# Performance work log

Hardware: AMD Instinct MI355X
Metric: run time of the kernel (lower is better)

The kernel has to match this reference:

```python
import jax, jax.numpy as jnp
import numpy as np

EPS = 1e-5

def _ln(x, g, b):
    m = x.mean(-1, keepdims=True)
    v = x.var(-1, keepdims=True)
    return (x - m) / jnp.sqrt(v + EPS) * g + b

def _dwconv(x, w, b, stride, pad):
    # x: [B,C,H,W], w: [C,1,k,k] depthwise
    C = x.shape[1]
    y = jax.lax.conv_general_dilated(
        x, w, (stride, stride), pad,
        feature_group_count=C,
        dimension_numbers=('NCHW', 'OIHW', 'NCHW'))
    return y + b[None, :, None, None]

def setup_inputs() -> dict:
    key = jax.random.key(0)
    ks = jax.random.split(key, 16)
    B, H, W, C = 8, 64, 64, 256
    N = H * W
    sr = 8
    d = {}
    d['x'] = jax.random.normal(ks[0], (B, N, C), jnp.float32)
    d['q_w'] = jax.random.normal(ks[1], (C, C), jnp.float32) * 0.02
    d['kv1_w'] = jax.random.normal(ks[2], (C, C), jnp.float32) * 0.02
    d['kv2_w'] = jax.random.normal(ks[3], (C, C), jnp.float32) * 0.02
    d['proj_w'] = jax.random.normal(ks[4], (C, C), jnp.float32) * 0.02
    d['proj_b'] = jnp.zeros((C,), jnp.float32)
    k1 = sr // 2
    d['sr1_w'] = jax.random.normal(ks[5], (C, 1, k1, k1), jnp.float32) * np.sqrt(2.0 / (k1 * k1))
    d['sr1_b'] = jnp.zeros((C,), jnp.float32)
    d['sr2_w'] = jax.random.normal(ks[6], (C, 1, sr, sr), jnp.float32) * np.sqrt(2.0 / (sr * sr))
    d['sr2_b'] = jnp.zeros((C,), jnp.float32)
    d['ln1_g'] = jnp.ones((C,), jnp.float32)
    d['ln1_b'] = jnp.zeros((C,), jnp.float32)
    d['ln2_g'] = jnp.ones((C,), jnp.float32)
    d['ln2_b'] = jnp.zeros((C,), jnp.float32)
    d['lc1_w'] = jax.random.normal(ks[7], (C // 2, 1, 3, 3), jnp.float32) * np.sqrt(2.0 / 9.0)
    d['lc1_b'] = jnp.zeros((C // 2,), jnp.float32)
    d['lc2_w'] = jax.random.normal(ks[8], (C // 2, 1, 3, 3), jnp.float32) * np.sqrt(2.0 / 9.0)
    d['lc2_b'] = jnp.zeros((C // 2,), jnp.float32)
    d['H'] = H
    d['W'] = W
    return d

def reference(x, q_w, kv1_w, kv2_w, proj_w, proj_b,
              sr1_w, sr1_b, sr2_w, sr2_b,
              ln1_g, ln1_b, ln2_g, ln2_b,
              lc1_w, lc1_b, lc2_w, lc2_b, H, W):
    B, N, C = x.shape
    nh = 8
    nh2 = nh // 2
    hd = C // nh
    sr = 8
    scale = hd ** -0.5

    # q: [B, nh, N, hd]
    q = jnp.einsum('bnc,dc->bnd', x, q_w).reshape(B, N, nh, hd).transpose(0, 2, 1, 3)

    x_ = x.transpose(0, 2, 1).reshape(B, C, H, W)
    x1 = _dwconv(x_, sr1_w, sr1_b, sr // 2, 'VALID')            # [B,C,H/4,W/4]
    x1 = x1.reshape(B, C, -1).transpose(0, 2, 1)                 # [B,N1,C]
    x1 = jax.nn.gelu(_ln(x1, ln1_g, ln1_b), approximate=False)
    x2 = _dwconv(x_, sr2_w, sr2_b, sr, 'VALID')                  # [B,C,H/8,W/8]
    x2 = x2.reshape(B, C, -1).transpose(0, 2, 1)                 # [B,N2,C]
    x2 = jax.nn.gelu(_ln(x2, ln2_g, ln2_b), approximate=False)

    def branch(xr, kv_w, qh, Hs, Ws, lc_w, lc_b):
        Bn, Ns, _ = xr.shape
        kv = jnp.einsum('bnc,dc->bnd', xr, kv_w).reshape(Bn, Ns, 2, nh2, hd).transpose(2, 0, 3, 1, 4)
        k, v = kv[0], kv[1]                                      # [B,nh2,Ns,hd]
        attn = jax.nn.softmax(jnp.einsum('bhqd,bhkd->bhqk', qh, k) * scale, axis=-1)
        # depthwise local conv injected into v
        v_sp = v.transpose(0, 2, 1, 3).reshape(Bn, Ns, C // 2).transpose(0, 2, 1).reshape(Bn, C // 2, Hs, Ws)
        v_lc = _dwconv(v_sp, lc_w, lc_b, 1, ((1, 1), (1, 1)))
        v = v + v_lc.reshape(Bn, nh2, hd, Ns).transpose(0, 1, 3, 2)
        out = jnp.einsum('bhqk,bhkd->bhqd', attn, v)             # [B,nh2,N,hd]
        return out.transpose(0, 2, 1, 3).reshape(Bn, N, C // 2)

    o1 = branch(x1, kv1_w, q[:, :nh2], H * 2 // sr, W * 2 // sr, lc1_w, lc1_b)
    o2 = branch(x2, kv2_w, q[:, nh2:], H // sr, W // sr, lc2_w, lc2_b)
    out = jnp.concatenate([o1, o2], axis=-1)
    return jnp.einsum('bnc,dc->bnd', out, proj_w) + proj_b
```

## Files before the change

kernel.cpp:

```cpp
#include <hip/hip_runtime.h>
#include <math.h>

static constexpr int Bb  = 8;
static constexpr int Nn  = 4096;
static constexpr int Cc  = 256;
static constexpr int N1c = 256;
static constexpr int N2c = 64;

typedef __attribute__((ext_vector_type(8))) _Float16 f16x8;
typedef __attribute__((ext_vector_type(4))) _Float16 f16x4;
typedef __attribute__((ext_vector_type(4))) float    f32x4v;

__global__ __launch_bounds__(256)
void prep_down(const float* __restrict__ w0, const float* __restrict__ w1,
               const float* __restrict__ w2, const float* __restrict__ w3,
               const float* __restrict__ x,
               const float* __restrict__ sr1w, const float* __restrict__ b1,
               const float* __restrict__ g1,   const float* __restrict__ lb1,
               const float* __restrict__ sr2w, const float* __restrict__ b2,
               const float* __restrict__ g2,   const float* __restrict__ lb2,
               _Float16* __restrict__ wf, _Float16* __restrict__ x1o,
               _Float16* __restrict__ x2o) {
  const int bid = blockIdx.x, c = threadIdx.x;
  if (bid < 256) {
    const int wsel = bid >> 6;
    const float* w = wsel == 0 ? w0 : wsel == 1 ? w1 : wsel == 2 ? w2 : w3;
    const int i = ((bid & 63) * 256 + c) * 4;
    float4 v = *(const float4*)(w + i);
    f16x4 o = {(_Float16)v.x, (_Float16)v.y, (_Float16)v.z, (_Float16)v.w};
    *(f16x4*)(wf + (size_t)wsel * 65536 + i) = o;
    return;
  }
  const int t = bid - 256;
  const int b = t >> 6, n2 = t & 63;
  const int i2 = n2 >> 3, j2 = n2 & 7;
  const int lane = c & 63, wave = c >> 6;
  const float* xb = x + ((size_t)b * Nn) * Cc + c;

  float w1r[16];
#pragma unroll
  for (int q = 0; q < 4; ++q)
    *(float4*)&w1r[4 * q] = *(const float4*)(sr1w + c * 16 + 4 * q);

  float a2 = b2[c];
  float a1[2][2] = {{b1[c], b1[c]}, {b1[c], b1[c]}};
#pragma unroll
  for (int dy = 0; dy < 8; ++dy) {
    float vr[8], w2r[8];
    *(float4*)&w2r[0] = *(const float4*)(sr2w + c * 64 + dy * 8);
    *(float4*)&w2r[4] = *(const float4*)(sr2w + c * 64 + dy * 8 + 4);
#pragma unroll
    for (int dx = 0; dx < 8; ++dx)
      vr[dx] = xb[(size_t)((8 * i2 + dy) * 64 + 8 * j2 + dx) * 256];
#pragma unroll
    for (int dx = 0; dx < 8; ++dx) {
      a2 = fmaf(w2r[dx], vr[dx], a2);
      a1[dy >> 2][dx >> 2] = fmaf(w1r[(dy & 3) * 4 + (dx & 3)], vr[dx],
                                  a1[dy >> 2][dx >> 2]);
    }
  }
  float vals[5] = {a2, a1[0][0], a1[0][1], a1[1][0], a1[1][1]};
  __shared__ float redS[4][5], redQ[4][5];
#pragma unroll
  for (int p = 0; p < 5; ++p) {
    float s = vals[p], q2 = vals[p] * vals[p];
#pragma unroll
    for (int off = 1; off < 64; off <<= 1) {
      s  += __shfl_xor(s, off);
      q2 += __shfl_xor(q2, off);
    }
    if (lane == 0) { redS[wave][p] = s; redQ[wave][p] = q2; }
  }
  __syncthreads();
#pragma unroll
  for (int p = 0; p < 5; ++p) {
    const float sum = redS[0][p] + redS[1][p] + redS[2][p] + redS[3][p];
    const float sq  = redQ[0][p] + redQ[1][p] + redQ[2][p] + redQ[3][p];
    const float mean = sum * (1.f / Cc);
    const float var  = sq * (1.f / Cc) - mean * mean;
    const float gg = (p == 0) ? g2[c] : g1[c];
    const float bb = (p == 0) ? lb2[c] : lb1[c];
    const float xn = (vals[p] - mean) * rsqrtf(var + 1e-5f) * gg + bb;
    const float gel = 0.5f * xn * (1.f + erff(xn * 0.70710678118654752440f));
    if (p == 0) {
      x2o[((size_t)b * N2c + n2) * 256 + c] = (_Float16)gel;
    } else {
      const int a = (p - 1) >> 1, bbx = (p - 1) & 1;
      const int n1 = (2 * i2 + a) * 16 + (2 * j2 + bbx);
      x1o[((size_t)b * N1c + n1) * 256 + c] = (_Float16)gel;
    }
  }
}

struct GemmSmem { _Float16 Asl[2][64][40]; _Float16 Bsl[2][256][40]; };

template<int AM, int OM, bool BIAS>
__device__ __forceinline__
void gemm_body(GemmSmem& sm, const void* __restrict__ Ain,
               const _Float16* __restrict__ Wf, const float* __restrict__ bias,
               void* __restrict__ Outv, int m0) {
  const int tid = threadIdx.x, lane = tid & 63, wid = tid >> 6;
  const int qi = lane & 15, g = lane >> 4;
  const int ar = tid >> 2, ak = (tid & 3) * 8;
  const int arow = m0 + ar;

  const float*    pa32 = (const float*)Ain + (size_t)arow * 256 + ak;
  const _Float16* pa16f = (const _Float16*)Ain + (size_t)arow * 256 + ak;
  const _Float16* pa16h = (const _Float16*)Ain
      + ((size_t)(arow >> 12) * 8 * 4096 + (arow & 4095)) * 32 + ak;
  const _Float16* pw = Wf + (size_t)tid * 256;

  f32x4v acc[4][4] = {};
  f16x8 rA; f16x8 rB[4];

#define LDREG(k0)                                                          \
  do {                                                                     \
    if (AM == 0) {                                                         \
      float4 t0 = *(const float4*)(pa32 + (k0));                           \
      float4 t1 = *(const float4*)(pa32 + (k0) + 4);                       \
      rA = (f16x8){(_Float16)t0.x, (_Float16)t0.y, (_Float16)t0.z,         \
                   (_Float16)t0.w, (_Float16)t1.x, (_Float16)t1.y,         \
                   (_Float16)t1.z, (_Float16)t1.w};                        \
    } else if (AM == 1) {                                                  \
      rA = *(const f16x8*)(pa16f + (k0));                                  \
    } else {                                                               \
      rA = *(const f16x8*)(pa16h + (size_t)((k0) >> 5) * 131072);          \
    }                                                                      \
    _Pragma("unroll")                                                      \
    for (int i = 0; i < 4; ++i) rB[i] = *(const f16x8*)(pw + (k0) + i * 8);\
  } while (0)

#define DSWRITE(buf)                                                       \
  do {                                                                     \
    *(f16x8*)&sm.Asl[buf][ar][ak] = rA;                                    \
    _Pragma("unroll")                                                      \
    for (int i = 0; i < 4; ++i) *(f16x8*)&sm.Bsl[buf][tid][i * 8] = rB[i]; \
  } while (0)

  LDREG(0);
  DSWRITE(0);
  LDREG(32);
  __syncthreads();

#pragma unroll
  for (int ks = 0; ks < 8; ++ks) {
    const int cur = ks & 1;
    if (ks < 7) DSWRITE(cur ^ 1);
    if (ks < 6) LDREG((ks + 2) * 32);
    f16x8 af[4], bf[4];
#pragma unroll
    for (int mt = 0; mt < 4; ++mt)
      af[mt] = *(const f16x8*)&sm.Asl[cur][mt * 16 + qi][g * 8];
#pragma unroll
    for (int nt = 0; nt < 4; ++nt)
      bf[nt] = *(const f16x8*)&sm.Bsl[cur][wid * 64 + nt * 16 + qi][g * 8];
#pragma unroll
    for (int nt = 0; nt < 4; ++nt)
#pragma unroll
      for (int mt = 0; mt < 4; ++mt)
        acc[mt][nt] = __builtin_amdgcn_mfma_f32_16x16x32_f16(af[mt], bf[nt], acc[mt][nt], 0, 0, 0);
    __syncthreads();
  }
#undef LDREG
#undef DSWRITE

#pragma unroll
  for (int nt = 0; nt < 4; ++nt) {
    const int col = wid * 64 + nt * 16 + qi;
    const float bv = BIAS ? bias[col] : 0.f;
    const int hs = col >> 5, d = col & 31;
#pragma unroll
    for (int mt = 0; mt < 4; ++mt) {
#pragma unroll
      for (int r = 0; r < 4; ++r) {
        const int row = m0 + mt * 16 + g * 4 + r;
        const float v = acc[mt][nt][r];
        if (OM == 0) {
          ((float*)Outv)[(size_t)row * 256 + col] = v + bv;
        } else if (OM == 1) {
          ((_Float16*)Outv)[((size_t)((row >> 12) * 8 + hs) * 4096 + (row & 4095)) * 32 + d] = (_Float16)v;
        } else if (OM == 2) {
          ((_Float16*)Outv)[((size_t)((row >> 8) * 8 + hs) * 256 + (row & 255)) * 32 + d] = (_Float16)v;
        } else {
          ((_Float16*)Outv)[((size_t)((row >> 6) * 8 + hs) * 64 + (row & 63)) * 32 + d] = (_Float16)v;
        }
      }
    }
  }
}

__global__ __launch_bounds__(256)
void gemms_qkv(const float* __restrict__ x, const _Float16* __restrict__ x1h,
               const _Float16* __restrict__ x2h, const _Float16* __restrict__ wf,
               _Float16* __restrict__ qh, _Float16* __restrict__ kv1,
               _Float16* __restrict__ kv2) {
  __shared__ GemmSmem sm;
  const int bx = blockIdx.x;
  if (bx < 512)      gemm_body<0, 1, false>(sm, x,   wf,             nullptr, qh,  bx * 64);
  else if (bx < 544) gemm_body<1, 2, false>(sm, x1h, wf + 65536,     nullptr, kv1, (bx - 512) * 64);
  else               gemm_body<1, 3, false>(sm, x2h, wf + 2 * 65536, nullptr, kv2, (bx - 544) * 64);
}

__global__ __launch_bounds__(256)
void gemm_proj(const _Float16* __restrict__ qh, const _Float16* __restrict__ wf,
               const float* __restrict__ bias, float* __restrict__ out) {
  __shared__ GemmSmem sm;
  gemm_body<2, 0, true>(sm, qh, wf, bias, out, blockIdx.x * 64);
}

template<int NS, int HS>
__device__ __forceinline__
void attn_body(char* smem, _Float16* __restrict__ qh, const _Float16* __restrict__ kvh,
               const float* __restrict__ lcw, const float* __restrict__ lcb,
               int qc, int b, int h, int hg) {
  constexpr int NT = NS / 16, NC = NS / 32, PS = NS + 8;
  constexpr float KC = 0.17677669529663688f * 1.4426950408889634f;
  _Float16 (*Klds)[40] = (_Float16(*)[40])smem;
  _Float16 (*Vt)[PS]   = (_Float16(*)[PS])(smem + (size_t)NS * 40 * 2);
  _Float16* PlBase     = (_Float16*)(smem + (size_t)NS * 40 * 2 + (size_t)32 * PS * 2);
  _Float16 (*vraw)[32] = (_Float16(*)[32])PlBase;

  const int tid = threadIdx.x, lane = tid & 63, wid = tid >> 6;
  const int g = lane >> 4, qi = lane & 15;

  const _Float16* kp0 = kvh + ((size_t)(b * 8 + h) * NS) * 32;
  const _Float16* vp0 = kvh + ((size_t)(b * 8 + 4 + h) * NS) * 32;
  for (int r = tid; r < NS; r += 256) {
#pragma unroll
    for (int i = 0; i < 4; ++i)
      *(f16x8*)&Klds[r][8 * i] = *(const f16x8*)(kp0 + (size_t)r * 32 + 8 * i);
#pragma unroll
    for (int i = 0; i < 4; ++i)
      *(f16x8*)&vraw[r][8 * i] = *(const f16x8*)(vp0 + (size_t)r * 32 + 8 * i);
  }
  __syncthreads();

  {
    const int d = tid & 31, rg = tid >> 5;
    const int cc = h * 32 + d;
    float wreg[9];
#pragma unroll
    for (int q = 0; q < 9; ++q) wreg[q] = lcw[cc * 9 + q];
    const float bv = lcb[cc];
    for (int r0 = rg; r0 < NS; r0 += 8) {
      const int i = r0 / HS, j = r0 % HS;
      float acc = bv;
#pragma unroll
      for (int dy = 0; dy < 3; ++dy) {
        const int ii = i + dy - 1;
        if (ii < 0 || ii >= HS) continue;
#pragma unroll
        for (int dx = 0; dx < 3; ++dx) {
          const int jj = j + dx - 1;
          if (jj < 0 || jj >= HS) continue;
          acc = fmaf(wreg[dy * 3 + dx], (float)vraw[ii * HS + jj][d], acc);
        }
      }
      Vt[d][r0] = (_Float16)((float)vraw[r0][d] + acc);
    }
  }
  __syncthreads();

  f16x8 vt[2][NC];
#pragma unroll
  for (int dt = 0; dt < 2; ++dt)
#pragma unroll
    for (int c = 0; c < NC; ++c)
      vt[dt][c] = *(const f16x8*)&Vt[16 * dt + qi][32 * c + 8 * g];

  _Float16* Pw = PlBase + (size_t)(wid * 16 + qi) * PS;
  _Float16* qbase = qh + ((size_t)(b * 8 + hg) * 4096) * 32;

  for (int qt = 0; qt < 4; ++qt) {
    const int qrow = qc * 256 + wid * 64 + qt * 16 + qi;
    _Float16* qp = qbase + (size_t)qrow * 32;
    f16x8 qfrag = *(const f16x8*)(qp + 8 * g);
    f32x4v s[NT];
#pragma unroll
    for (int t = 0; t < NT; ++t) {
      f16x8 kf = *(const f16x8*)&Klds[16 * t + qi][8 * g];
      s[t] = __builtin_amdgcn_mfma_f32_16x16x32_f16(kf, qfrag,
                                                    (f32x4v){0.f, 0.f, 0.f, 0.f}, 0, 0, 0);
    }
    float m = s[0][0];
#pragma unroll
    for (int t = 0; t < NT; ++t)
      m = fmaxf(m, fmaxf(fmaxf(s[t][0], s[t][1]), fmaxf(s[t][2], s[t][3])));
    m = fmaxf(m, __shfl_xor(m, 16));
    m = fmaxf(m, __shfl_xor(m, 32));
    float l = 0.f;
#pragma unroll
    for (int t = 0; t < NT; ++t)
#pragma unroll
      for (int r = 0; r < 4; ++r) {
        float p = exp2f((s[t][r] - m) * KC);
        s[t][r] = p; l += p;
      }
    l += __shfl_xor(l, 16);
    l += __shfl_xor(l, 32);
#pragma unroll
    for (int t = 0; t < NT; ++t) {
      f16x4 pw = {(_Float16)s[t][0], (_Float16)s[t][1],
                  (_Float16)s[t][2], (_Float16)s[t][3]};
      *(f16x4*)&Pw[16 * t + 4 * g] = pw;
    }
    f32x4v o0 = {0.f, 0.f, 0.f, 0.f}, o1 = {0.f, 0.f, 0.f, 0.f};
#pragma unroll
    for (int c = 0; c < NC; ++c) {
      f16x8 pf = *(const f16x8*)&Pw[32 * c + 8 * g];
      o0 = __builtin_amdgcn_mfma_f32_16x16x32_f16(vt[0][c], pf, o0, 0, 0, 0);
      o1 = __builtin_amdgcn_mfma_f32_16x16x32_f16(vt[1][c], pf, o1, 0, 0, 0);
    }
    const float inv = 1.f / l;
    f16x4 O0 = {(_Float16)(o0[0] * inv), (_Float16)(o0[1] * inv),
                (_Float16)(o0[2] * inv), (_Float16)(o0[3] * inv)};
    f16x4 O1 = {(_Float16)(o1[0] * inv), (_Float16)(o1[1] * inv),
                (_Float16)(o1[2] * inv), (_Float16)(o1[3] * inv)};
    *(f16x4*)(qp + 4 * g)      = O0;
    *(f16x4*)(qp + 16 + 4 * g) = O1;
  }
}

__global__ __launch_bounds__(256, 2)
void attn_all(_Float16* __restrict__ qh,
              const _Float16* __restrict__ kv1, const _Float16* __restrict__ kv2,
              const float* __restrict__ lc1w, const float* __restrict__ lc1b,
              const float* __restrict__ lc2w, const float* __restrict__ lc2b) {
  __shared__ __align__(16) char smem[71168];
  const int z = blockIdx.z;
  const int b = z >> 1, br = z & 1;
  const int h = blockIdx.y;
  if (br == 0) attn_body<256, 16>(smem, qh, kv1, lc1w, lc1b, blockIdx.x, b, h, h);
  else         attn_body<64,  8>(smem, qh, kv2, lc2w, lc2b, blockIdx.x, b, h, 4 + h);
}

extern "C" void kernel_launch(void* const* d_in, const int* in_sizes, int n_in,
                              void* d_out, int out_size, void* d_ws, size_t ws_size,
                              hipStream_t stream) {
  const float* x      = (const float*)d_in[0];
  const float* q_w    = (const float*)d_in[1];
  const float* kv1_w  = (const float*)d_in[2];
  const float* kv2_w  = (const float*)d_in[3];
  const float* proj_w = (const float*)d_in[4];
  const float* proj_b = (const float*)d_in[5];
  const float* sr1_w  = (const float*)d_in[6];
  const float* sr1_b  = (const float*)d_in[7];
  const float* sr2_w  = (const float*)d_in[8];
  const float* sr2_b  = (const float*)d_in[9];
  const float* ln1_g  = (const float*)d_in[10];
  const float* ln1_b  = (const float*)d_in[11];
  const float* ln2_g  = (const float*)d_in[12];
  const float* ln2_b  = (const float*)d_in[13];
  const float* lc1_w  = (const float*)d_in[14];
  const float* lc1_b  = (const float*)d_in[15];
  const float* lc2_w  = (const float*)d_in[16];
  const float* lc2_b  = (const float*)d_in[17];
  float* out = (float*)d_out;

  _Float16* wf   = (_Float16*)d_ws;
  _Float16* qh   = wf + (size_t)4 * 65536;
  _Float16* x1h  = qh + (size_t)Bb * Nn * Cc;
  _Float16* x2h  = x1h + (size_t)Bb * N1c * Cc;
  _Float16* kv1h = x2h + (size_t)Bb * N2c * Cc;
  _Float16* kv2h = kv1h + (size_t)Bb * N1c * Cc;

  prep_down<<<768, 256, 0, stream>>>(q_w, kv1_w, kv2_w, proj_w, x,
                                     sr1_w, sr1_b, ln1_g, ln1_b,
                                     sr2_w, sr2_b, ln2_g, ln2_b,
                                     wf, x1h, x2h);
  gemms_qkv<<<552, 256, 0, stream>>>(x, x1h, x2h, wf, qh, kv1h, kv2h);
  attn_all<<<dim3(16, 4, 16), 256, 0, stream>>>(qh, kv1h, kv2h,
                                                lc1_w, lc1_b, lc2_w, lc2_b);
  gemm_proj<<<512, 256, 0, stream>>>(qh, wf + 3 * 65536, proj_b, out);
}
```

Before: 106.1 us.

## Precompute depthwise-conv V transpose in separate kernel, shrink attention LDS

Moves the 3x3 depthwise local conv on V, plus its transpose, out of every attention block into a small dedicated kernel that writes a transposed V buffer to global memory once per (batch, head). Previously each of the 16 query-chunk blocks recomputed the same conv. The attention kernel now just loads the precomputed Vt, aliases the P buffer over Vt after an extra barrier, and cuts shared memory from about 71KB to 54KB so it can raise the occupancy hint to 3 blocks. The cost is an extra kernel launch and an extra global round trip for V.

```diff
diff --git a/kernel.cpp b/kernel.cpp
--- a/kernel.cpp
+++ b/kernel.cpp
@@ -210,53 +210,79 @@
 
 template<int NS, int HS>
 __device__ __forceinline__
+void vconvt_body(const _Float16* __restrict__ kvh, const float* __restrict__ lcw,
+                 const float* __restrict__ lcb, _Float16* __restrict__ vtg,
+                 int b, int h, int rbase) {
+  const int tid = threadIdx.x;
+  const int r = rbase + (tid >> 2), dp = tid & 3, d0 = dp * 8;
+  const int i = r / HS, j = r % HS;
+  const _Float16* vsrc = kvh + ((size_t)(b * 8 + 4 + h) * NS) * 32;
+  const float* wb = lcw + (h * 32 + d0) * 9;
+  float acc[8];
+#pragma unroll
+  for (int e = 0; e < 8; ++e) acc[e] = lcb[h * 32 + d0 + e];
+#pragma unroll
+  for (int dy = 0; dy < 3; ++dy) {
+    const int ii = i + dy - 1;
+    if (ii < 0 || ii >= HS) continue;
+#pragma unroll
+    for (int dx = 0; dx < 3; ++dx) {
+      const int jj = j + dx - 1;
+      if (jj < 0 || jj >= HS) continue;
+      f16x8 v = *(const f16x8*)(vsrc + (size_t)(ii * HS + jj) * 32 + d0);
+#pragma unroll
+      for (int e = 0; e < 8; ++e)
+        acc[e] = fmaf(wb[e * 9 + dy * 3 + dx], (float)v[e], acc[e]);
+    }
+  }
+  f16x8 self = *(const f16x8*)(vsrc + (size_t)r * 32 + d0);
+  _Float16* dst = vtg + ((size_t)(b * 4 + h) * 32 + d0) * NS + r;
+#pragma unroll
+  for (int e = 0; e < 8; ++e)
+    dst[(size_t)e * NS] = (_Float16)(acc[e] + (float)self[e]);
+}
+
+__global__ __launch_bounds__(256)
+void vconv_t(const _Float16* __restrict__ kv1, const _Float16* __restrict__ kv2,
+             const float* __restrict__ lc1w, const float* __restrict__ lc1b,
+             const float* __restrict__ lc2w, const float* __restrict__ lc2b,
+             _Float16* __restrict__ vt1, _Float16* __restrict__ vt2) {
+  const int bid = blockIdx.x;
+  if (bid < 128) {
+    const int b = bid >> 4, h = (bid >> 2) & 3, rc = bid & 3;
+    vconvt_body<256, 16>(kv1, lc1w, lc1b, vt1, b, h, rc * 64);
+  } else {
+    const int t = bid - 128;
+    vconvt_body<64, 8>(kv2, lc2w, lc2b, vt2, t >> 2, t & 3, 0);
+  }
+}
+
+template<int NS, int HS>
+__device__ __forceinline__
 void attn_body(char* smem, _Float16* __restrict__ qh, const _Float16* __restrict__ kvh,
-               const float* __restrict__ lcw, const float* __restrict__ lcb,
-               int qc, int b, int h, int hg) {
+               const _Float16* __restrict__ vtg, int qc, int b, int h, int hg) {
   constexpr int NT = NS / 16, NC = NS / 32, PS = NS + 8;
   constexpr float KC = 0.17677669529663688f * 1.4426950408889634f;
   _Float16 (*Klds)[40] = (_Float16(*)[40])smem;
-  _Float16 (*Vt)[PS]   = (_Float16(*)[PS])(smem + (size_t)NS * 40 * 2);
-  _Float16* PlBase     = (_Float16*)(smem + (size_t)NS * 40 * 2 + (size_t)32 * PS * 2);
-  _Float16 (*vraw)[32] = (_Float16(*)[32])PlBase;
+  char* ubase = smem + (size_t)NS * 40 * 2;
+  _Float16 (*Vt)[PS]  = (_Float16(*)[PS])ubase;
+  _Float16* PlBase    = (_Float16*)ubase;
 
   const int tid = threadIdx.x, lane = tid & 63, wid = tid >> 6;
   const int g = lane >> 4, qi = lane & 15;
 
   const _Float16* kp0 = kvh + ((size_t)(b * 8 + h) * NS) * 32;
-  const _Float16* vp0 = kvh + ((size_t)(b * 8 + 4 + h) * NS) * 32;
   for (int r = tid; r < NS; r += 256) {
 #pragma unroll
     for (int i = 0; i < 4; ++i)
       *(f16x8*)&Klds[r][8 * i] = *(const f16x8*)(kp0 + (size_t)r * 32 + 8 * i);
-#pragma unroll
-    for (int i = 0; i < 4; ++i)
-      *(f16x8*)&vraw[r][8 * i] = *(const f16x8*)(vp0 + (size_t)r * 32 + 8 * i);
-  }
-  __syncthreads();
-
+  }
   {
-    const int d = tid & 31, rg = tid >> 5;
-    const int cc = h * 32 + d;
-    float wreg[9];
-#pragma unroll
-    for (int q = 0; q < 9; ++q) wreg[q] = lcw[cc * 9 + q];
-    const float bv = lcb[cc];
-    for (int r0 = rg; r0 < NS; r0 += 8) {
-      const int i = r0 / HS, j = r0 % HS;
-      float acc = bv;
-#pragma unroll
-      for (int dy = 0; dy < 3; ++dy) {
-        const int ii = i + dy - 1;
-        if (ii < 0 || ii >= HS) continue;
-#pragma unroll
-        for (int dx = 0; dx < 3; ++dx) {
-          const int jj = j + dx - 1;
-          if (jj < 0 || jj >= HS) continue;
-          acc = fmaf(wreg[dy * 3 + dx], (float)vraw[ii * HS + jj][d], acc);
-        }
-      }
-      Vt[d][r0] = (_Float16)((float)vraw[r0][d] + acc);
+    const _Float16* vg = vtg + ((size_t)(b * 4 + h) * 32) * NS;
+    constexpr int CPR = NS / 8;
+    for (int u = tid; u < 32 * CPR; u += 256) {
+      const int d = u / CPR, cj = u % CPR;
+      *(f16x8*)&Vt[d][cj * 8] = *(const f16x8*)(vg + (size_t)d * NS + cj * 8);
     }
   }
   __syncthreads();
@@ -267,6 +293,7 @@
 #pragma unroll
     for (int c = 0; c < NC; ++c)
       vt[dt][c] = *(const f16x8*)&Vt[16 * dt + qi][32 * c + 8 * g];
+  __syncthreads();
 
   _Float16* Pw = PlBase + (size_t)(wid * 16 + qi) * PS;
   _Float16* qbase = qh + ((size_t)(b * 8 + hg) * 4096) * 32;
@@ -321,17 +348,16 @@
   }
 }
 
-__global__ __launch_bounds__(256, 2)
+__global__ __launch_bounds__(256, 3)
 void attn_all(_Float16* __restrict__ qh,
               const _Float16* __restrict__ kv1, const _Float16* __restrict__ kv2,
-              const float* __restrict__ lc1w, const float* __restrict__ lc1b,
-              const float* __restrict__ lc2w, const float* __restrict__ lc2b) {
-  __shared__ __align__(16) char smem[71168];
+              const _Float16* __restrict__ vt1, const _Float16* __restrict__ vt2) {
+  __shared__ __align__(16) char smem[54272];
   const int z = blockIdx.z;
   const int b = z >> 1, br = z & 1;
   const int h = blockIdx.y;
-  if (br == 0) attn_body<256, 16>(smem, qh, kv1, lc1w, lc1b, blockIdx.x, b, h, h);
-  else         attn_body<64,  8>(smem, qh, kv2, lc2w, lc2b, blockIdx.x, b, h, 4 + h);
+  if (br == 0) attn_body<256, 16>(smem, qh, kv1, vt1, blockIdx.x, b, h, h);
+  else         attn_body<64,  8>(smem, qh, kv2, vt2, blockIdx.x, b, h, 4 + h);
 }
 
 extern "C" void kernel_launch(void* const* d_in, const int* in_sizes, int n_in,
@@ -363,13 +389,15 @@
   _Float16* x2h  = x1h + (size_t)Bb * N1c * Cc;
   _Float16* kv1h = x2h + (size_t)Bb * N2c * Cc;
   _Float16* kv2h = kv1h + (size_t)Bb * N1c * Cc;
+  _Float16* vt1  = kv2h + (size_t)Bb * N2c * Cc;
+  _Float16* vt2  = vt1  + (size_t)Bb * 4 * 32 * N1c;
 
   prep_down<<<768, 256, 0, stream>>>(q_w, kv1_w, kv2_w, proj_w, x,
                                      sr1_w, sr1_b, ln1_g, ln1_b,
                                      sr2_w, sr2_b, ln2_g, ln2_b,
                                      wf, x1h, x2h);
   gemms_qkv<<<552, 256, 0, stream>>>(x, x1h, x2h, wf, qh, kv1h, kv2h);
-  attn_all<<<dim3(16, 4, 16), 256, 0, stream>>>(qh, kv1h, kv2h,
-                                                lc1_w, lc1_b, lc2_w, lc2_b);
+  vconv_t<<<160, 256, 0, stream>>>(kv1h, kv2h, lc1_w, lc1_b, lc2_w, lc2_b, vt1, vt2);
+  attn_all<<<dim3(16, 4, 16), 256, 0, stream>>>(qh, kv1h, kv2h, vt1, vt2);
   gemm_proj<<<512, 256, 0, stream>>>(qh, wf + 3 * 65536, proj_b, out);
 }
```

Result: faster. 88.46 us (-16.6%).

## Emit fp16 copy of x in downsample pass; restructure attention V-conv and tiling

Applied to the files above, without the earlier changes.

The downsample kernel, which already reads every element of x, now also writes an fp16 copy of x. The Q GEMM reads that copy instead of converting fp32 x itself. The attention kernel stops staging raw V in LDS: the depthwise 3x3 conv reads V directly from global memory, eight channels per thread, and the P buffer shares LDS with Vt. This shrinks LDS per block so occupancy can go to 3 blocks per CU. Each block now handles twice as many query rows with half the grid, which adds an extra fp16 write of x and more global reads in the conv in exchange.

```diff
diff --git a/kernel.cpp b/kernel.cpp
--- a/kernel.cpp
+++ b/kernel.cpp
@@ -20,7 +20,7 @@
                const float* __restrict__ sr2w, const float* __restrict__ b2,
                const float* __restrict__ g2,   const float* __restrict__ lb2,
                _Float16* __restrict__ wf, _Float16* __restrict__ x1o,
-               _Float16* __restrict__ x2o) {
+               _Float16* __restrict__ x2o, _Float16* __restrict__ xh) {
   const int bid = blockIdx.x, c = threadIdx.x;
   if (bid < 256) {
     const int wsel = bid >> 6;
@@ -36,6 +36,7 @@
   const int i2 = n2 >> 3, j2 = n2 & 7;
   const int lane = c & 63, wave = c >> 6;
   const float* xb = x + ((size_t)b * Nn) * Cc + c;
+  _Float16* xhb = xh + ((size_t)b * Nn) * Cc + c;
 
   float w1r[16];
 #pragma unroll
@@ -50,8 +51,11 @@
     *(float4*)&w2r[0] = *(const float4*)(sr2w + c * 64 + dy * 8);
     *(float4*)&w2r[4] = *(const float4*)(sr2w + c * 64 + dy * 8 + 4);
 #pragma unroll
-    for (int dx = 0; dx < 8; ++dx)
-      vr[dx] = xb[(size_t)((8 * i2 + dy) * 64 + 8 * j2 + dx) * 256];
+    for (int dx = 0; dx < 8; ++dx) {
+      const int n = (8 * i2 + dy) * 64 + 8 * j2 + dx;
+      vr[dx] = xb[(size_t)n * 256];
+      xhb[(size_t)n * 256] = (_Float16)vr[dx];
+    }
 #pragma unroll
     for (int dx = 0; dx < 8; ++dx) {
       a2 = fmaf(w2r[dx], vr[dx], a2);
@@ -104,7 +108,6 @@
   const int ar = tid >> 2, ak = (tid & 3) * 8;
   const int arow = m0 + ar;
 
-  const float*    pa32 = (const float*)Ain + (size_t)arow * 256 + ak;
   const _Float16* pa16f = (const _Float16*)Ain + (size_t)arow * 256 + ak;
   const _Float16* pa16h = (const _Float16*)Ain
       + ((size_t)(arow >> 12) * 8 * 4096 + (arow & 4095)) * 32 + ak;
@@ -115,13 +118,7 @@
 
 #define LDREG(k0)                                                          \
   do {                                                                     \
-    if (AM == 0) {                                                         \
-      float4 t0 = *(const float4*)(pa32 + (k0));                           \
-      float4 t1 = *(const float4*)(pa32 + (k0) + 4);                       \
-      rA = (f16x8){(_Float16)t0.x, (_Float16)t0.y, (_Float16)t0.z,         \
-                   (_Float16)t0.w, (_Float16)t1.x, (_Float16)t1.y,         \
-                   (_Float16)t1.z, (_Float16)t1.w};                        \
-    } else if (AM == 1) {                                                  \
+    if (AM == 1) {                                                         \
       rA = *(const f16x8*)(pa16f + (k0));                                  \
     } else {                                                               \
       rA = *(const f16x8*)(pa16h + (size_t)((k0) >> 5) * 131072);          \
@@ -190,13 +187,13 @@
 }
 
 __global__ __launch_bounds__(256)
-void gemms_qkv(const float* __restrict__ x, const _Float16* __restrict__ x1h,
+void gemms_qkv(const _Float16* __restrict__ xh, const _Float16* __restrict__ x1h,
                const _Float16* __restrict__ x2h, const _Float16* __restrict__ wf,
                _Float16* __restrict__ qh, _Float16* __restrict__ kv1,
                _Float16* __restrict__ kv2) {
   __shared__ GemmSmem sm;
   const int bx = blockIdx.x;
-  if (bx < 512)      gemm_body<0, 1, false>(sm, x,   wf,             nullptr, qh,  bx * 64);
+  if (bx < 512)      gemm_body<1, 1, false>(sm, xh,  wf,             nullptr, qh,  bx * 64);
   else if (bx < 544) gemm_body<1, 2, false>(sm, x1h, wf + 65536,     nullptr, kv1, (bx - 512) * 64);
   else               gemm_body<1, 3, false>(sm, x2h, wf + 2 * 65536, nullptr, kv2, (bx - 544) * 64);
 }
@@ -216,35 +213,35 @@
   constexpr int NT = NS / 16, NC = NS / 32, PS = NS + 8;
   constexpr float KC = 0.17677669529663688f * 1.4426950408889634f;
   _Float16 (*Klds)[40] = (_Float16(*)[40])smem;
-  _Float16 (*Vt)[PS]   = (_Float16(*)[PS])(smem + (size_t)NS * 40 * 2);
-  _Float16* PlBase     = (_Float16*)(smem + (size_t)NS * 40 * 2 + (size_t)32 * PS * 2);
-  _Float16 (*vraw)[32] = (_Float16(*)[32])PlBase;
+  char* ubase = smem + (size_t)NS * 40 * 2;
+  _Float16 (*Vt)[PS]  = (_Float16(*)[PS])ubase;
+  _Float16* PlBase    = (_Float16*)ubase;
 
   const int tid = threadIdx.x, lane = tid & 63, wid = tid >> 6;
   const int g = lane >> 4, qi = lane & 15;
 
   const _Float16* kp0 = kvh + ((size_t)(b * 8 + h) * NS) * 32;
-  const _Float16* vp0 = kvh + ((size_t)(b * 8 + 4 + h) * NS) * 32;
   for (int r = tid; r < NS; r += 256) {
 #pragma unroll
     for (int i = 0; i < 4; ++i)
       *(f16x8*)&Klds[r][8 * i] = *(const f16x8*)(kp0 + (size_t)r * 32 + 8 * i);
-#pragma unroll
-    for (int i = 0; i < 4; ++i)
-      *(f16x8*)&vraw[r][8 * i] = *(const f16x8*)(vp0 + (size_t)r * 32 + 8 * i);
-  }
-  __syncthreads();
+  }
 
   {
-    const int d = tid & 31, rg = tid >> 5;
-    const int cc = h * 32 + d;
-    float wreg[9];
-#pragma unroll
-    for (int q = 0; q < 9; ++q) wreg[q] = lcw[cc * 9 + q];
-    const float bv = lcb[cc];
-    for (int r0 = rg; r0 < NS; r0 += 8) {
+    const int dp = tid & 3, d0 = dp * 8;
+    const _Float16* vsrc = kvh + ((size_t)(b * 8 + 4 + h) * NS) * 32;
+    float wreg[72];
+    const float* wq = lcw + (size_t)(h * 32 + d0) * 9;
+#pragma unroll
+    for (int i = 0; i < 72; ++i) wreg[i] = wq[i];
+    float bvv[8];
+#pragma unroll
+    for (int e = 0; e < 8; ++e) bvv[e] = lcb[h * 32 + d0 + e];
+    for (int r0 = tid >> 2; r0 < NS; r0 += 64) {
       const int i = r0 / HS, j = r0 % HS;
-      float acc = bv;
+      float acc[8];
+#pragma unroll
+      for (int e = 0; e < 8; ++e) acc[e] = bvv[e];
 #pragma unroll
       for (int dy = 0; dy < 3; ++dy) {
         const int ii = i + dy - 1;
@@ -253,10 +250,16 @@
         for (int dx = 0; dx < 3; ++dx) {
           const int jj = j + dx - 1;
           if (jj < 0 || jj >= HS) continue;
-          acc = fmaf(wreg[dy * 3 + dx], (float)vraw[ii * HS + jj][d], acc);
+          f16x8 v = *(const f16x8*)(vsrc + (size_t)(ii * HS + jj) * 32 + d0);
+#pragma unroll
+          for (int e = 0; e < 8; ++e)
+            acc[e] = fmaf(wreg[e * 9 + dy * 3 + dx], (float)v[e], acc[e]);
         }
       }
-      Vt[d][r0] = (_Float16)((float)vraw[r0][d] + acc);
+      f16x8 self = *(const f16x8*)(vsrc + (size_t)r0 * 32 + d0);
+#pragma unroll
+      for (int e = 0; e < 8; ++e)
+        Vt[d0 + e][r0] = (_Float16)(acc[e] + (float)self[e]);
     }
   }
   __syncthreads();
@@ -267,12 +270,13 @@
 #pragma unroll
     for (int c = 0; c < NC; ++c)
       vt[dt][c] = *(const f16x8*)&Vt[16 * dt + qi][32 * c + 8 * g];
+  __syncthreads();
 
   _Float16* Pw = PlBase + (size_t)(wid * 16 + qi) * PS;
   _Float16* qbase = qh + ((size_t)(b * 8 + hg) * 4096) * 32;
 
-  for (int qt = 0; qt < 4; ++qt) {
-    const int qrow = qc * 256 + wid * 64 + qt * 16 + qi;
+  for (int qt = 0; qt < 8; ++qt) {
+    const int qrow = qc * 512 + wid * 128 + qt * 16 + qi;
     _Float16* qp = qbase + (size_t)qrow * 32;
     f16x8 qfrag = *(const f16x8*)(qp + 8 * g);
     f32x4v s[NT];
@@ -321,12 +325,12 @@
   }
 }
 
-__global__ __launch_bounds__(256, 2)
+__global__ __launch_bounds__(256, 3)
 void attn_all(_Float16* __restrict__ qh,
               const _Float16* __restrict__ kv1, const _Float16* __restrict__ kv2,
               const float* __restrict__ lc1w, const float* __restrict__ lc1b,
               const float* __restrict__ lc2w, const float* __restrict__ lc2b) {
-  __shared__ __align__(16) char smem[71168];
+  __shared__ __align__(16) char smem[54272];
   const int z = blockIdx.z;
   const int b = z >> 1, br = z & 1;
   const int h = blockIdx.y;
@@ -363,13 +367,14 @@
   _Float16* x2h  = x1h + (size_t)Bb * N1c * Cc;
   _Float16* kv1h = x2h + (size_t)Bb * N2c * Cc;
   _Float16* kv2h = kv1h + (size_t)Bb * N1c * Cc;
+  _Float16* xh   = kv2h + (size_t)Bb * N2c * Cc;
 
   prep_down<<<768, 256, 0, stream>>>(q_w, kv1_w, kv2_w, proj_w, x,
                                      sr1_w, sr1_b, ln1_g, ln1_b,
                                      sr2_w, sr2_b, ln2_g, ln2_b,
-                                     wf, x1h, x2h);
-  gemms_qkv<<<552, 256, 0, stream>>>(x, x1h, x2h, wf, qh, kv1h, kv2h);
-  attn_all<<<dim3(16, 4, 16), 256, 0, stream>>>(qh, kv1h, kv2h,
-                                                lc1_w, lc1_b, lc2_w, lc2_b);
+                                     wf, x1h, x2h, xh);
+  gemms_qkv<<<552, 256, 0, stream>>>(xh, x1h, x2h, wf, qh, kv1h, kv2h);
+  attn_all<<<dim3(8, 4, 16), 256, 0, stream>>>(qh, kv1h, kv2h,
+                                               lc1_w, lc1_b, lc2_w, lc2_b);
   gemm_proj<<<512, 256, 0, stream>>>(qh, wf + 3 * 65536, proj_b, out);
 }
```

New measurement: 96.68 us. -8.9%, faster.
